# Performance work log

Measured on AMD Instinct MI355X. Metric: run time of the kernel, lower is better.

The kernel has to match this reference:

```python
import jax, jax.numpy as jnp
import numpy as np

E = 2048
H = 16
D = E // H  # head_dim = 128
S_SLOTS = 8
EPS = 1e-5


def _linear_params(key, fan_in, fan_out):
    kw, kb = jax.random.split(key)
    lim = 1.0 / np.sqrt(fan_in)
    W = jax.random.uniform(kw, (fan_out, fan_in), jnp.float32, -lim, lim)
    b = jax.random.uniform(kb, (fan_out,), jnp.float32, -lim, lim)
    return W, b


def setup_inputs() -> dict:
    key = jax.random.key(0)
    ks = jax.random.split(key, 10)
    x = jax.random.normal(ks[0], (2, 2048, E), jnp.float32)
    thought_slots = jax.random.normal(ks[1], (S_SLOTS, E), jnp.float32)
    Wq, bq = _linear_params(ks[2], E, E)
    Wk, bk = _linear_params(ks[3], E, E)
    Wv, bv = _linear_params(ks[4], E, E)
    Wtq, btq = _linear_params(ks[5], E, E)
    Wtk, btk = _linear_params(ks[6], E, E)
    Wtv, btv = _linear_params(ks[7], E, E)
    Wo, bo = _linear_params(ks[8], E, E)
    gamma = jnp.ones((E,), jnp.float32)
    beta = jnp.zeros((E,), jnp.float32)
    return dict(x=x, thought_slots=thought_slots, Wq=Wq, bq=bq, Wk=Wk, bk=bk,
                Wv=Wv, bv=bv, Wtq=Wtq, btq=btq, Wtk=Wtk, btk=btk,
                Wtv=Wtv, btv=btv, Wo=Wo, bo=bo, gamma=gamma, beta=beta)


def _heads(t, B):
    # [B, S, E] -> [B, H, S, D]
    return t.reshape(B, -1, H, D).transpose(0, 2, 1, 3)


def reference(x, thought_slots, Wq, bq, Wk, bk, Wv, bv,
              Wtq, btq, Wtk, btk, Wtv, btv, Wo, bo, gamma, beta):
    B, S, _ = x.shape
    scale = 1.0 / np.sqrt(D)

    # regular self-attention stream
    q = _heads(x @ Wq.T + bq, B)
    k = _heads(x @ Wk.T + bk, B)
    v = _heads(x @ Wv.T + bv, B)
    attn = jax.nn.softmax(jnp.einsum('bhqd,bhkd->bhqk', q, k) * scale, axis=-1)
    regular_out = jnp.einsum('bhqk,bhkd->bhqd', attn, v)

    # thought cross-attention stream (keys/values from learned slots)
    slots = jnp.broadcast_to(thought_slots, (B, S_SLOTS, thought_slots.shape[-1]))
    t_q = _heads(x @ Wtq.T + btq, B)
    t_k = _heads(slots @ Wtk.T + btk, B)
    t_v = _heads(slots @ Wtv.T + btv, B)
    t_attn = jax.nn.softmax(jnp.einsum('bhqd,bhkd->bhqk', t_q, t_k) * scale, axis=-1)
    thought_out = jnp.einsum('bhqk,bhkd->bhqd', t_attn, t_v)

    # merge heads, combine, layernorm, output projection
    combined = (regular_out + thought_out).transpose(0, 2, 1, 3).reshape(B, S, E)
    mu = jnp.mean(combined, axis=-1, keepdims=True)
    var = jnp.var(combined, axis=-1, keepdims=True)
    normed = (combined - mu) * jax.lax.rsqrt(var + EPS) * gamma + beta
    return normed @ Wo.T + bo
```

## Files before the change

### kernel.cpp

```cpp
#include <hip/hip_runtime.h>
#include <hip/hip_bf16.h>
#include <stdint.h>

typedef __bf16 bf16;
typedef __bf16 bf16x8 __attribute__((ext_vector_type(8)));
typedef __bf16 bf16x4 __attribute__((ext_vector_type(4)));
typedef float f32x4 __attribute__((ext_vector_type(4)));
typedef float f32x16 __attribute__((ext_vector_type(16)));
typedef uint32_t u32x2 __attribute__((ext_vector_type(2)));
typedef uint32_t u32x4 __attribute__((ext_vector_type(4)));

#define E_DIM 2048
#define HEADS 16
#define HD 128
#define SEQ 2048
#define BATCH 2
#define NTOK 4096
#define NSLOT 8

#define QSCALE (0.08838834764831845f * 1.4426950408889634f)

#define WAITV(N) asm volatile("s_waitcnt vmcnt(" #N ")" ::: "memory")

__device__ __forceinline__ void gload_lds16(const void* g, void* lds) {
  __builtin_amdgcn_global_load_lds(
      (const __attribute__((address_space(1))) uint32_t*)g,
      (__attribute__((address_space(3))) uint32_t*)lds, 16, 0, 0);
}

__global__ __launch_bounds__(256) void cvt_f32_bf16_kernel(
    const float* __restrict__ src, bf16* __restrict__ dst, int n8)
{
  for (int i = blockIdx.x * 256 + threadIdx.x; i < n8; i += gridDim.x * 256) {
    const f32x4 a = *(const f32x4*)(src + i * 8);
    const f32x4 b = *(const f32x4*)(src + i * 8 + 4);
    bf16x8 o;
#pragma unroll
    for (int j = 0; j < 4; j++) { o[j] = (bf16)a[j]; o[4 + j] = (bf16)b[j]; }
    *(bf16x8*)(dst + i * 8) = o;
  }
}

struct CvtArgs { const float* src[5]; bf16* dst[5]; };

__global__ __launch_bounds__(256) void cvt5_kernel(CvtArgs a, int n8)
{
  const float* __restrict__ src = a.src[blockIdx.y];
  bf16* __restrict__ dst = a.dst[blockIdx.y];
  for (int i = blockIdx.x * 256 + threadIdx.x; i < n8; i += gridDim.x * 256) {
    const f32x4 x = *(const f32x4*)(src + i * 8);
    const f32x4 y = *(const f32x4*)(src + i * 8 + 4);
    bf16x8 o;
#pragma unroll
    for (int j = 0; j < 4; j++) { o[j] = (bf16)x[j]; o[4 + j] = (bf16)y[j]; }
    *(bf16x8*)(dst + i * 8) = o;
  }
}

struct ProjArgs {
  const bf16* W[4];
  const float* bias[4];
  void* out[4];
  int mode[4];
  float scale[4];
};

__global__ __launch_bounds__(512, 2) void gemm256_kernel(
    const bf16* __restrict__ A, ProjArgs pa, int nbm, int nbn)
{
  __shared__ char As_[2 * 32768];
  __shared__ char Bs_[2 * 32768];

  const int nwg = gridDim.x;
  const int qch = nwg >> 3;
  const int wg = (blockIdx.x & 7) * qch + (blockIdx.x >> 3);
  const int bm = wg % nbm;
  const int rest = wg / nbm;
  const int bn = rest % nbn;
  const int z = rest / nbn;

  const bf16* __restrict__ W = pa.W[z];
  const float* __restrict__ bias = pa.bias[z];
  void* __restrict__ out = pa.out[z];
  const int mode = pa.mode[z];
  const float scale = pa.scale[z];

  const int tid = threadIdx.x;
  const int lane = tid & 63;
  const int w = tid >> 6;
  const int wr = w >> 2;
  const int wc = w & 3;
  const int g = lane >> 4, c = lane & 15;

  const int srow = tid >> 3;
  const int sslot = tid & 7;
  const int scol = (sslot ^ (srow & 7)) * 8;
  const bf16* Abase = A + (size_t)(bm * 256) * 2048;
  const bf16* Bbase = W + (size_t)(bn * 256) * 2048;

  auto stageU = [&](const bf16* gbase, char* lds, int T, int u) {
    char* dst = lds + (T & 1) * 32768 + u * 16384;
    const int k0 = T * 64;
#pragma unroll
    for (int j = 0; j < 2; j++) {
      const int r = u * 128 + srow + j * 64;
      gload_lds16(gbase + (size_t)r * 2048 + k0 + scol,
                  dst + (size_t)(srow + j * 64) * 128 + sslot * 16);
    }
  };

  f32x4 acc[8][4] = {};
  bf16x8 bfr[4][2];

  stageU(Bbase, Bs_, 0, 0); stageU(Bbase, Bs_, 0, 1);
  stageU(Abase, As_, 0, 0); stageU(Abase, As_, 0, 1);
  stageU(Bbase, Bs_, 1, 0); stageU(Bbase, Bs_, 1, 1);
  stageU(Abase, As_, 1, 0);
  WAITV(6);
  __builtin_amdgcn_s_barrier();

  const int NT = 2048 / 64;
  for (int t = 0; t < NT; t++) {
    const int d = t & 1;
    const char* Aq = As_ + d * 32768;
    const char* Bq = Bs_ + d * 32768;
#pragma unroll
    for (int q = 0; q < 4; q++) {
      bf16x8 af[2][2];
      if (q == 0) {
#pragma unroll
        for (int n = 0; n < 4; n++)
#pragma unroll
          for (int kk = 0; kk < 2; kk++) {
            const int row = wc * 64 + n * 16 + c;
            bfr[n][kk] = *(const bf16x8*)(Bq + (size_t)row * 128 +
                                          (((kk * 4 + g) ^ (c & 7)) * 16));
          }
      }
#pragma unroll
      for (int mi2 = 0; mi2 < 2; mi2++)
#pragma unroll
        for (int kk = 0; kk < 2; kk++) {
          const int row = wr * 128 + (q * 2 + mi2) * 16 + c;
          af[mi2][kk] = *(const bf16x8*)(Aq + (size_t)row * 128 +
                                         (((kk * 4 + g) ^ (c & 7)) * 16));
        }

      if (q == 0)      { if (t + 1 < NT) stageU(Abase, As_, t + 1, 1); }
      else if (q == 1) { if (t + 2 < NT) stageU(Bbase, Bs_, t + 2, 0); }
      else if (q == 2) { if (t + 2 < NT) stageU(Bbase, Bs_, t + 2, 1); }
      else {
        __builtin_amdgcn_s_barrier();
        if (t + 2 < NT) stageU(Abase, As_, t + 2, 0);
      }

      __builtin_amdgcn_s_setprio(1);
#pragma unroll
      for (int mi2 = 0; mi2 < 2; mi2++)
#pragma unroll
        for (int n = 0; n < 4; n++)
#pragma unroll
          for (int kk = 0; kk < 2; kk++)
            acc[q * 2 + mi2][n] = __builtin_amdgcn_mfma_f32_16x16x32_bf16(
                af[mi2][kk], bfr[n][kk], acc[q * 2 + mi2][n], 0, 0, 0);
      __builtin_amdgcn_s_setprio(0);

      if (q == 0) {
        __builtin_amdgcn_s_barrier();
      } else if (q == 3) {
        if (t < NT - 2)       { WAITV(6); }
        else if (t == NT - 2) { WAITV(0); }
        __builtin_amdgcn_s_barrier();
      }
    }
  }

#pragma unroll
  for (int mi = 0; mi < 8; mi++) {
#pragma unroll
    for (int n = 0; n < 4; n++) {
      const int col = bn * 256 + wc * 64 + n * 16 + c;
      const float bv = bias[col];
#pragma unroll
      for (int j = 0; j < 4; j++) {
        const int row = bm * 256 + wr * 128 + mi * 16 + g * 4 + j;
        const float v = (acc[mi][n][j] + bv) * scale;
        if (mode == 0) {
          ((float*)out)[(size_t)row * E_DIM + col] = v;
        } else {
          const int b = row >> 11, s = row & 2047;
          const int h = col >> 7, d2 = col & 127;
          size_t idx;
          if (mode == 1) idx = (((size_t)(b * HEADS + h)) * SEQ + s) * HD + d2;
          else           idx = (((size_t)(b * HEADS + h)) * HD + d2) * SEQ + s;
          ((bf16*)out)[idx] = (bf16)v;
        }
      }
    }
  }
}

__global__ __launch_bounds__(256) void gemm_nt_kernel(
    const bf16* __restrict__ A, ProjArgs pa, int M, int N, int K)
{
  __shared__ bf16 As[2][128 * 32];
  __shared__ bf16 Bs[2][128 * 32];

  const int z = blockIdx.z;
  const bf16* __restrict__ W = pa.W[z];
  const float* __restrict__ bias = pa.bias[z];
  void* __restrict__ out = pa.out[z];
  const int mode = pa.mode[z];
  const float scale = pa.scale[z];

  const int tid = threadIdx.x;
  const int lane = tid & 63;
  const int w = tid >> 6;
  const int wr = w >> 1, wc = w & 1;
  const int g = lane >> 4, c = lane & 15;
  const int bm = blockIdx.x, bn = blockIdx.y;

  f32x4 acc[4][4] = {};

  const int srow = lane >> 2;
  const int scol = (lane & 3) * 8;
  const bf16* Ab = A + (size_t)(bm * 128 + srow) * K + scol;
  const bf16* Wb = W + (size_t)(bn * 128 + srow) * K + scol;

  auto stage = [&](int k0, int buf) {
#pragma unroll
    for (int i = 0; i < 2; ++i) {
      const int chunk = w * 2 + i;
      gload_lds16(Ab + (size_t)(chunk * 16) * K + k0, (char*)(&As[buf][0]) + chunk * 1024);
      gload_lds16(Wb + (size_t)(chunk * 16) * K + k0, (char*)(&Bs[buf][0]) + chunk * 1024);
    }
  };

  stage(0, 0);
  __syncthreads();
  int cur = 0;

  for (int k0 = 0; k0 < K; k0 += 32) {
    if (k0 + 32 < K) stage(k0 + 32, cur ^ 1);
    bf16x8 af[4], bfr[4];
#pragma unroll
    for (int m = 0; m < 4; m++)
      af[m] = *(const bf16x8*)(&As[cur][0] + (wr * 64 + m * 16 + c) * 32 + g * 8);
#pragma unroll
    for (int n = 0; n < 4; n++)
      bfr[n] = *(const bf16x8*)(&Bs[cur][0] + (wc * 64 + n * 16 + c) * 32 + g * 8);
#pragma unroll
    for (int m = 0; m < 4; m++)
#pragma unroll
      for (int n = 0; n < 4; n++)
        acc[m][n] = __builtin_amdgcn_mfma_f32_16x16x32_bf16(af[m], bfr[n], acc[m][n], 0, 0, 0);
    __syncthreads();
    cur ^= 1;
  }

#pragma unroll
  for (int m = 0; m < 4; m++) {
#pragma unroll
    for (int n = 0; n < 4; n++) {
      const int col = bn * 128 + wc * 64 + n * 16 + c;
      const float bv = bias[col];
#pragma unroll
      for (int j = 0; j < 4; j++) {
        const int row = bm * 128 + wr * 64 + m * 16 + g * 4 + j;
        const float v = (acc[m][n][j] + bv) * scale;
        if (mode == 0) {
          ((float*)out)[(size_t)row * N + col] = v;
        } else {
          const int b = row >> 11, s = row & 2047;
          const int h = col >> 7, d = col & 127;
          size_t idx;
          if (mode == 1) idx = (((size_t)(b * HEADS + h)) * SEQ + s) * HD + d;
          else           idx = (((size_t)(b * HEADS + h)) * HD + d) * SEQ + s;
          ((bf16*)out)[idx] = (bf16)v;
        }
      }
    }
  }
}

__global__ __launch_bounds__(256) void slots_proj_kernel(
    const float* __restrict__ slots,
    const float* __restrict__ Wk, const float* __restrict__ bk,
    const float* __restrict__ Wv, const float* __restrict__ bv,
    float* __restrict__ tk, float* __restrict__ tv)
{
  const int col = blockIdx.x * 256 + threadIdx.x;
  const int slot = blockIdx.y;
  const int mat = blockIdx.z;
  const float* W = mat ? Wv : Wk;
  const float* bias = mat ? bv : bk;
  float* out = mat ? tv : tk;
  const float* xr = slots + (size_t)slot * E_DIM;
  const float* wr = W + (size_t)col * E_DIM;
  float acc = 0.f;
  for (int k = 0; k < E_DIM; k += 4) {
    const f32x4 a = *(const f32x4*)(xr + k);
    const f32x4 b4 = *(const f32x4*)(wr + k);
#pragma unroll
    for (int i = 0; i < 4; i++) acc += a[i] * b4[i];
  }
  out[(size_t)slot * E_DIM + col] = acc + bias[col];
}

__global__ __launch_bounds__(512) void flash_attn_kernel(
    const bf16* __restrict__ Qg, const bf16* __restrict__ Kg,
    const bf16* __restrict__ Vtg, bf16* __restrict__ Og)
{
  __shared__ char Ks[3][64 * 256];
  __shared__ char Vs[3][128 * 128];

  const int orig = blockIdx.x;
  const int logical = (orig & 7) * 32 + (orig >> 3);
  const int qt = logical & 7;
  const int bh = logical >> 3;

  const int tid = threadIdx.x;
  const int lane = tid & 63;
  const int w = tid >> 6;
  const int q = lane & 31;
  const int hi = lane >> 5;
  const int b = bh >> 4, h = bh & 15;
  const int q0 = qt * 256 + w * 32;

  const bf16* Qb = Qg + ((size_t)bh * SEQ + q0) * HD;
  const bf16* Kb = Kg + (size_t)bh * SEQ * HD;
  const bf16* Vb = Vtg + (size_t)bh * HD * SEQ;

  auto stage = [&](int kv0, int buf) {
#pragma unroll
    for (int i = 0; i < 2; i++) {
      const int p = (tid + i * 512) * 16;
      { const int r = p >> 8; const int s16 = (p >> 4) & 15;
        gload_lds16(Kb + (size_t)(kv0 + r) * HD + (s16 ^ (r & 15)) * 8, &Ks[0][0] + buf * 16384 + p); }
      { const int r = p >> 7; const int s8 = (p >> 4) & 7;
        gload_lds16(Vb + (size_t)r * SEQ + kv0 + (s8 ^ (r & 7)) * 8, &Vs[0][0] + buf * 16384 + p); }
    }
  };

  bf16x8 qf[8];
#pragma unroll
  for (int kc = 0; kc < 8; kc++)
    qf[kc] = *(const bf16x8*)(Qb + (size_t)q * HD + kc * 16 + hi * 8);

  f32x16 o[4] = {};
  float mrun = -1e30f, lsum = 0.f;
  bf16x8 pbo[2][2];

  stage(0, 0);
  __syncthreads();

  int prv = 2, cur = 0, nxt = 1;
  const int NT = SEQ / 64;

  for (int t = 0; t < NT; t++) {
    if (t + 1 < NT) stage((t + 1) * 64, nxt);

    f32x16 st[2] = {};
    const char* Kc = &Ks[0][0] + cur * 16384;
    __builtin_amdgcn_s_setprio(1);
#pragma unroll
    for (int kc = 0; kc < 8; kc++) {
#pragma unroll
      for (int blk = 0; blk < 2; blk++) {
        const int rt = blk * 32 + q;
        const int sl = (2 * kc + hi) ^ (rt & 15);
        const bf16x8 kf = *(const bf16x8*)(Kc + rt * 256 + sl * 16);
        st[blk] = __builtin_amdgcn_mfma_f32_32x32x16_bf16(kf, qf[kc], st[blk], 0, 0, 0);
      }
    }
    __builtin_amdgcn_s_setprio(0);

    float tm[16];
#pragma unroll
    for (int i = 0; i < 16; i++) tm[i] = fmaxf(st[0][i], st[1][i]);
#pragma unroll
    for (int s2 = 8; s2 > 0; s2 >>= 1)
#pragma unroll
      for (int i = 0; i < 8; i++) if (i < s2) tm[i] = fmaxf(tm[i], tm[i + s2]);
    float lm = tm[0];
    lm = fmaxf(lm, __shfl_xor(lm, 32));
    float fsc = 1.0f;
    const bool resc = __any(lm > mrun + 8.0f);
    if (resc) {
      const float mn = fmaxf(mrun, lm);
      fsc = exp2f(mrun - mn);
      mrun = mn;
    }

    float ps0 = 0.f, ps1 = 0.f, ps2 = 0.f, ps3 = 0.f;
#pragma unroll
    for (int blk = 0; blk < 2; blk++)
#pragma unroll
      for (int i = 0; i < 16; i += 4) {
        const float p0 = exp2f(st[blk][i]     - mrun);
        const float p1 = exp2f(st[blk][i + 1] - mrun);
        const float p2 = exp2f(st[blk][i + 2] - mrun);
        const float p3 = exp2f(st[blk][i + 3] - mrun);
        st[blk][i] = p0; st[blk][i + 1] = p1; st[blk][i + 2] = p2; st[blk][i + 3] = p3;
        ps0 += p0; ps1 += p1; ps2 += p2; ps3 += p3;
      }
    lsum = lsum * fsc + ((ps0 + ps1) + (ps2 + ps3));

    bf16x8 pbn[2][2];
#pragma unroll
    for (int blk = 0; blk < 2; blk++)
#pragma unroll
      for (int c2 = 0; c2 < 2; c2++) {
        bf16x4 Lv, Hv;
#pragma unroll
        for (int i = 0; i < 4; i++) {
          Lv[i] = (bf16)st[blk][8 * c2 + i];
          Hv[i] = (bf16)st[blk][8 * c2 + 4 + i];
        }
        const u32x2 Lu = __builtin_bit_cast(u32x2, Lv);
        const u32x2 Hu = __builtin_bit_cast(u32x2, Hv);
        const uint32_t s0 = hi ? Lu.x : Hu.x;
        const uint32_t s1 = hi ? Lu.y : Hu.y;
        const uint32_t x0 = (uint32_t)__shfl_xor((int)s0, 32);
        const uint32_t x1 = (uint32_t)__shfl_xor((int)s1, 32);
        u32x4 bv;
        bv.x = hi ? x0 : Lu.x;
        bv.y = hi ? x1 : Lu.y;
        bv.z = hi ? Hu.x : x0;
        bv.w = hi ? Hu.y : x1;
        pbn[blk][c2] = __builtin_bit_cast(bf16x8, bv);
      }

    if (t > 0) {
      const char* Vc = &Vs[0][0] + prv * 16384;
#pragma unroll
      for (int db = 0; db < 4; db++) {
        const int rt = db * 32 + q;
#pragma unroll
        for (int blk = 0; blk < 2; blk++)
#pragma unroll
          for (int c2 = 0; c2 < 2; c2++) {
            const int sl = (blk * 4 + c2 * 2 + hi) ^ (rt & 7);
            const bf16x8 vf = *(const bf16x8*)(Vc + rt * 128 + sl * 16);
            o[db] = __builtin_amdgcn_mfma_f32_32x32x16_bf16(vf, pbo[blk][c2], o[db], 0, 0, 0);
          }
      }
    }

    if (resc) {
#pragma unroll
      for (int db = 0; db < 4; db++)
#pragma unroll
        for (int i = 0; i < 16; i++) o[db][i] *= fsc;
    }

#pragma unroll
    for (int blk = 0; blk < 2; blk++)
#pragma unroll
      for (int c2 = 0; c2 < 2; c2++) pbo[blk][c2] = pbn[blk][c2];

    __syncthreads();
    const int tmp = prv; prv = cur; cur = nxt; nxt = tmp;
  }

  {
    const char* Vc = &Vs[0][0] + prv * 16384;
#pragma unroll
    for (int db = 0; db < 4; db++) {
      const int rt = db * 32 + q;
#pragma unroll
      for (int blk = 0; blk < 2; blk++)
#pragma unroll
        for (int c2 = 0; c2 < 2; c2++) {
          const int sl = (blk * 4 + c2 * 2 + hi) ^ (rt & 7);
          const bf16x8 vf = *(const bf16x8*)(Vc + rt * 128 + sl * 16);
          o[db] = __builtin_amdgcn_mfma_f32_32x32x16_bf16(vf, pbo[blk][c2], o[db], 0, 0, 0);
        }
    }
  }

  const float lt = lsum + __shfl_xor(lsum, 32);
  const float linv = 1.0f / lt;
  bf16* Orow = Og + ((size_t)b * SEQ + q0 + q) * E_DIM + h * HD;
#pragma unroll
  for (int db = 0; db < 4; db++)
#pragma unroll
    for (int g4 = 0; g4 < 4; g4++) {
      bf16x4 ov;
#pragma unroll
      for (int i = 0; i < 4; i++) ov[i] = (bf16)(o[db][g4 * 4 + i] * linv);
      *(bf16x4*)(Orow + db * 32 + g4 * 8 + hi * 4) = ov;
    }
}

__global__ __launch_bounds__(256) void thought_ln_kernel(
    const bf16* __restrict__ TQ, const float* __restrict__ TK,
    const float* __restrict__ TV, const bf16* __restrict__ ATT,
    const float* __restrict__ gamma, const float* __restrict__ beta,
    bf16* __restrict__ Y)
{
  __shared__ float wsum[4], wsq[4];
  const int tid = threadIdx.x;
  const int lane = tid & 63;
  const int w = tid >> 6;
  const int tok = blockIdx.x;
  const int b = tok >> 11, s = tok & 2047;
  const int e0 = tid * 8;
  const int h = e0 >> 7;
  const int d0 = e0 & 127;

  const bf16x8 av = *(const bf16x8*)(ATT + (size_t)tok * E_DIM + e0);
  float v[8];
#pragma unroll
  for (int i = 0; i < 8; i++) v[i] = (float)av[i];

  const bf16x8 qv8 = *(const bf16x8*)(TQ + (((size_t)(b * HEADS + h)) * SEQ + s) * HD + d0);
  float qv[8];
#pragma unroll
  for (int i = 0; i < 8; i++) qv[i] = (float)qv8[i];

  float dts[NSLOT];
#pragma unroll
  for (int sl = 0; sl < NSLOT; sl++) {
    const float* tkr = TK + (size_t)sl * E_DIM + e0;
    const f32x4 k0 = *(const f32x4*)(tkr);
    const f32x4 k1 = *(const f32x4*)(tkr + 4);
    float dp = 0.f;
#pragma unroll
    for (int i = 0; i < 4; i++) dp += qv[i] * k0[i] + qv[4 + i] * k1[i];
    dp += __shfl_xor(dp, 1);
    dp += __shfl_xor(dp, 2);
    dp += __shfl_xor(dp, 4);
    dp += __shfl_xor(dp, 8);
    dts[sl] = dp;
  }
  float mx = dts[0];
#pragma unroll
  for (int sl = 1; sl < NSLOT; sl++) mx = fmaxf(mx, dts[sl]);
  float p[NSLOT], den = 0.f;
#pragma unroll
  for (int sl = 0; sl < NSLOT; sl++) { p[sl] = exp2f(dts[sl] - mx); den += p[sl]; }
  const float dinv = 1.0f / den;
#pragma unroll
  for (int sl = 0; sl < NSLOT; sl++) {
    const float pn = p[sl] * dinv;
    const float* tvr = TV + (size_t)sl * E_DIM + e0;
    const f32x4 v0 = *(const f32x4*)(tvr);
    const f32x4 v1 = *(const f32x4*)(tvr + 4);
#pragma unroll
    for (int i = 0; i < 4; i++) { v[i] += pn * v0[i]; v[4 + i] += pn * v1[i]; }
  }

  float sm = 0.f, sq = 0.f;
#pragma unroll
  for (int i = 0; i < 8; i++) { sm += v[i]; sq += v[i] * v[i]; }
#pragma unroll
  for (int d = 1; d < 64; d <<= 1) { sm += __shfl_xor(sm, d); sq += __shfl_xor(sq, d); }
  if (lane == 0) { wsum[w] = sm; wsq[w] = sq; }
  __syncthreads();
  const float ts = wsum[0] + wsum[1] + wsum[2] + wsum[3];
  const float tq2 = wsq[0] + wsq[1] + wsq[2] + wsq[3];
  const float mean = ts * (1.f / E_DIM);
  const float var = tq2 * (1.f / E_DIM) - mean * mean;
  const float rstd = rsqrtf(var + 1e-5f);
  const f32x4 g0 = *(const f32x4*)(gamma + e0);
  const f32x4 g1 = *(const f32x4*)(gamma + e0 + 4);
  const f32x4 b0 = *(const f32x4*)(beta + e0);
  const f32x4 b1 = *(const f32x4*)(beta + e0 + 4);
  bf16x8 outv;
#pragma unroll
  for (int i = 0; i < 4; i++) {
    outv[i]     = (bf16)((v[i]     - mean) * rstd * g0[i] + b0[i]);
    outv[4 + i] = (bf16)((v[4 + i] - mean) * rstd * g1[i] + b1[i]);
  }
  *(bf16x8*)(Y + (size_t)tok * E_DIM + e0) = outv;
}

extern "C" void kernel_launch(void* const* d_in, const int* in_sizes, int n_in,
                              void* d_out, int out_size, void* d_ws, size_t ws_size,
                              hipStream_t stream) {
  (void)in_sizes; (void)n_in; (void)out_size; (void)ws_size;
  const float* x     = (const float*)d_in[0];
  const float* slots = (const float*)d_in[1];
  const float* Wq  = (const float*)d_in[2];   const float* bq  = (const float*)d_in[3];
  const float* Wk  = (const float*)d_in[4];   const float* bk  = (const float*)d_in[5];
  const float* Wv  = (const float*)d_in[6];   const float* bv  = (const float*)d_in[7];
  const float* Wtq = (const float*)d_in[8];   const float* btq = (const float*)d_in[9];
  const float* Wtk = (const float*)d_in[10];  const float* btk = (const float*)d_in[11];
  const float* Wtv = (const float*)d_in[12];  const float* btv = (const float*)d_in[13];
  const float* Wo  = (const float*)d_in[14];  const float* bo  = (const float*)d_in[15];
  const float* gamma = (const float*)d_in[16];
  const float* beta  = (const float*)d_in[17];

  uint8_t* ws = (uint8_t*)d_ws;
  const size_t BUF  = (size_t)NTOK * E_DIM * sizeof(bf16);
  const size_t WBUF = (size_t)E_DIM * E_DIM * sizeof(bf16);
  bf16* xb   = (bf16*)(ws + 0 * BUF);
  bf16* qb   = (bf16*)(ws + 1 * BUF);
  bf16* kb   = (bf16*)(ws + 2 * BUF);
  bf16* vtb  = (bf16*)(ws + 3 * BUF);
  bf16* tqb  = (bf16*)(ws + 4 * BUF);
  bf16* attb = (bf16*)(ws + 5 * BUF);
  bf16* nrmb = qb;
  uint8_t* wp = ws + 6 * BUF;
  bf16* Wqb  = (bf16*)(wp + 0 * WBUF);
  bf16* Wkb  = (bf16*)(wp + 1 * WBUF);
  bf16* Wvb  = (bf16*)(wp + 2 * WBUF);
  bf16* Wtqb = (bf16*)(wp + 3 * WBUF);
  bf16* Wob  = (bf16*)(wp + 4 * WBUF);
  float* tkb = (float*)(wp + 5 * WBUF);
  float* tvb = (float*)(wp + 5 * WBUF + 128 * 1024);

  const int WN8 = E_DIM * E_DIM / 8;
  const int XN8 = NTOK * E_DIM / 8;
  cvt_f32_bf16_kernel<<<dim3(2048), 256, 0, stream>>>(x, xb, XN8);
  CvtArgs ca;
  ca.src[0] = Wq;  ca.dst[0] = Wqb;
  ca.src[1] = Wk;  ca.dst[1] = Wkb;
  ca.src[2] = Wv;  ca.dst[2] = Wvb;
  ca.src[3] = Wtq; ca.dst[3] = Wtqb;
  ca.src[4] = Wo;  ca.dst[4] = Wob;
  cvt5_kernel<<<dim3(1024, 5), 256, 0, stream>>>(ca, WN8);

  ProjArgs pa;
  pa.W[0] = Wqb;  pa.bias[0] = bq;  pa.out[0] = qb;  pa.mode[0] = 1; pa.scale[0] = QSCALE;
  pa.W[1] = Wkb;  pa.bias[1] = bk;  pa.out[1] = kb;  pa.mode[1] = 1; pa.scale[1] = 1.0f;
  pa.W[2] = Wvb;  pa.bias[2] = bv;  pa.out[2] = vtb; pa.mode[2] = 2; pa.scale[2] = 1.0f;
  pa.W[3] = Wtqb; pa.bias[3] = btq; pa.out[3] = tqb; pa.mode[3] = 1; pa.scale[3] = QSCALE;
  gemm256_kernel<<<dim3(16 * 8 * 4), 512, 0, stream>>>(xb, pa, 16, 8);

  slots_proj_kernel<<<dim3(E_DIM / 256, NSLOT, 2), 256, 0, stream>>>(
      slots, Wtk, btk, Wtv, btv, tkb, tvb);

  flash_attn_kernel<<<dim3((SEQ / 256) * BATCH * HEADS), 512, 0, stream>>>(
      qb, kb, vtb, attb);
  thought_ln_kernel<<<dim3(NTOK), 256, 0, stream>>>(
      tqb, tkb, tvb, attb, gamma, beta, nrmb);

  ProjArgs po;
  po.W[0] = Wob; po.bias[0] = bo; po.out[0] = d_out; po.mode[0] = 0; po.scale[0] = 1.0f;
  po.W[1] = po.W[2] = po.W[3] = Wob;
  po.bias[1] = po.bias[2] = po.bias[3] = bo;
  po.out[1] = po.out[2] = po.out[3] = d_out;
  po.mode[1] = po.mode[2] = po.mode[3] = 0;
  po.scale[1] = po.scale[2] = po.scale[3] = 1.0f;
  gemm_nt_kernel<<<dim3(NTOK / 128, E_DIM / 128, 1), 256, 0, stream>>>(
      nrmb, po, NTOK, E_DIM, E_DIM);
}
```

Baseline: 432.0 us.

## Replace output projection with split-K 256-tile GEMM and bias reduction

The output projection no longer uses the small 128x128-tile GEMM. It now runs a 256x256-tile kernel with split-K of 2 over 256 workgroups, remapped across XCDs. Each half writes bf16 partials into reused workspace buffers, and a separate kernel sums them, adds the bias and writes the fp32 output. The A-tile staging order and LDS layout are also changed, and the barrier placement is adjusted in the main QKV GEMM loop. The aim is better MFMA utilisation and more occupancy for the last GEMM, at the cost of an extra partial round-trip through memory and bf16 rounding of the partials.

```diff
diff --git a/kernel.cpp b/kernel.cpp
--- a/kernel.cpp
+++ b/kernel.cpp
@@ -98,13 +98,23 @@
   const bf16* Abase = A + (size_t)(bm * 256) * 2048;
   const bf16* Bbase = W + (size_t)(bn * 256) * 2048;
 
-  auto stageU = [&](const bf16* gbase, char* lds, int T, int u) {
-    char* dst = lds + (T & 1) * 32768 + u * 16384;
+  auto stageB = [&](int T, int u) {
+    char* dst = Bs_ + (T & 1) * 32768 + u * 16384;
     const int k0 = T * 64;
 #pragma unroll
     for (int j = 0; j < 2; j++) {
       const int r = u * 128 + srow + j * 64;
-      gload_lds16(gbase + (size_t)r * 2048 + k0 + scol,
+      gload_lds16(Bbase + (size_t)r * 2048 + k0 + scol,
+                  dst + (size_t)(srow + j * 64) * 128 + sslot * 16);
+    }
+  };
+  auto stageA = [&](int T, int u) {
+    char* dst = As_ + (T & 1) * 32768 + u * 16384;
+    const int k0 = T * 64;
+#pragma unroll
+    for (int j = 0; j < 2; j++) {
+      const int r = j * 128 + u * 64 + srow;
+      gload_lds16(Abase + (size_t)r * 2048 + k0 + scol,
                   dst + (size_t)(srow + j * 64) * 128 + sslot * 16);
     }
   };
@@ -112,10 +122,8 @@
   f32x4 acc[8][4] = {};
   bf16x8 bfr[4][2];
 
-  stageU(Bbase, Bs_, 0, 0); stageU(Bbase, Bs_, 0, 1);
-  stageU(Abase, As_, 0, 0); stageU(Abase, As_, 0, 1);
-  stageU(Bbase, Bs_, 1, 0); stageU(Bbase, Bs_, 1, 1);
-  stageU(Abase, As_, 1, 0);
+  stageB(0, 0); stageB(0, 1); stageA(0, 0); stageA(0, 1);
+  stageB(1, 0); stageB(1, 1); stageA(1, 0);
   WAITV(6);
   __builtin_amdgcn_s_barrier();
 
@@ -142,17 +150,15 @@
 #pragma unroll
         for (int kk = 0; kk < 2; kk++) {
           const int row = wr * 128 + (q * 2 + mi2) * 16 + c;
-          af[mi2][kk] = *(const bf16x8*)(Aq + (size_t)row * 128 +
+          const int slab = (row >> 6) & 1;
+          const int aoff = (row & 63) + ((row >> 7) << 6);
+          af[mi2][kk] = *(const bf16x8*)(Aq + slab * 16384 + (size_t)aoff * 128 +
                                          (((kk * 4 + g) ^ (c & 7)) * 16));
         }
 
-      if (q == 0)      { if (t + 1 < NT) stageU(Abase, As_, t + 1, 1); }
-      else if (q == 1) { if (t + 2 < NT) stageU(Bbase, Bs_, t + 2, 0); }
-      else if (q == 2) { if (t + 2 < NT) stageU(Bbase, Bs_, t + 2, 1); }
-      else {
-        __builtin_amdgcn_s_barrier();
-        if (t + 2 < NT) stageU(Abase, As_, t + 2, 0);
-      }
+      if (q == 0)      { if (t + 1 < NT) stageA(t + 1, 1); }
+      else if (q == 2) { if (t + 2 < NT) stageB(t + 2, 0); }
+      else if (q == 3) { if (t + 2 < NT) { stageB(t + 2, 1); stageA(t + 2, 0); } }
 
       __builtin_amdgcn_s_setprio(1);
 #pragma unroll
@@ -165,7 +171,7 @@
                 af[mi2][kk], bfr[n][kk], acc[q * 2 + mi2][n], 0, 0, 0);
       __builtin_amdgcn_s_setprio(0);
 
-      if (q == 0) {
+      if (q == 1) {
         __builtin_amdgcn_s_barrier();
       } else if (q == 3) {
         if (t < NT - 2)       { WAITV(6); }
@@ -185,101 +191,162 @@
       for (int j = 0; j < 4; j++) {
         const int row = bm * 256 + wr * 128 + mi * 16 + g * 4 + j;
         const float v = (acc[mi][n][j] + bv) * scale;
-        if (mode == 0) {
-          ((float*)out)[(size_t)row * E_DIM + col] = v;
-        } else {
-          const int b = row >> 11, s = row & 2047;
-          const int h = col >> 7, d2 = col & 127;
-          size_t idx;
-          if (mode == 1) idx = (((size_t)(b * HEADS + h)) * SEQ + s) * HD + d2;
-          else           idx = (((size_t)(b * HEADS + h)) * HD + d2) * SEQ + s;
-          ((bf16*)out)[idx] = (bf16)v;
-        }
-      }
-    }
-  }
-}
-
-__global__ __launch_bounds__(256) void gemm_nt_kernel(
-    const bf16* __restrict__ A, ProjArgs pa, int M, int N, int K)
+        const int b = row >> 11, s = row & 2047;
+        const int h = col >> 7, d2 = col & 127;
+        size_t idx;
+        if (mode == 1) idx = (((size_t)(b * HEADS + h)) * SEQ + s) * HD + d2;
+        else           idx = (((size_t)(b * HEADS + h)) * HD + d2) * SEQ + s;
+        ((bf16*)out)[idx] = (bf16)v;
+      }
+    }
+  }
+}
+
+__global__ __launch_bounds__(512, 2) void gemm256k_kernel(
+    const bf16* __restrict__ A, const bf16* __restrict__ W,
+    bf16* __restrict__ P0, bf16* __restrict__ P1)
 {
-  __shared__ bf16 As[2][128 * 32];
-  __shared__ bf16 Bs[2][128 * 32];
-
-  const int z = blockIdx.z;
-  const bf16* __restrict__ W = pa.W[z];
-  const float* __restrict__ bias = pa.bias[z];
-  void* __restrict__ out = pa.out[z];
-  const int mode = pa.mode[z];
-  const float scale = pa.scale[z];
+  __shared__ char As_[2 * 32768];
+  __shared__ char Bs_[2 * 32768];
+
+  const int nwg = gridDim.x;
+  const int qch = nwg >> 3;
+  const int wg = (blockIdx.x & 7) * qch + (blockIdx.x >> 3);
+  const int bm = wg % 16;
+  const int rest = wg / 16;
+  const int bn = rest & 7;
+  const int ks = rest >> 3;
+  bf16* __restrict__ out = ks ? P1 : P0;
+  const int kbase = ks * 1024;
 
   const int tid = threadIdx.x;
   const int lane = tid & 63;
   const int w = tid >> 6;
-  const int wr = w >> 1, wc = w & 1;
+  const int wr = w >> 2;
+  const int wc = w & 3;
   const int g = lane >> 4, c = lane & 15;
-  const int bm = blockIdx.x, bn = blockIdx.y;
-
-  f32x4 acc[4][4] = {};
-
-  const int srow = lane >> 2;
-  const int scol = (lane & 3) * 8;
-  const bf16* Ab = A + (size_t)(bm * 128 + srow) * K + scol;
-  const bf16* Wb = W + (size_t)(bn * 128 + srow) * K + scol;
-
-  auto stage = [&](int k0, int buf) {
-#pragma unroll
-    for (int i = 0; i < 2; ++i) {
-      const int chunk = w * 2 + i;
-      gload_lds16(Ab + (size_t)(chunk * 16) * K + k0, (char*)(&As[buf][0]) + chunk * 1024);
-      gload_lds16(Wb + (size_t)(chunk * 16) * K + k0, (char*)(&Bs[buf][0]) + chunk * 1024);
+
+  const int srow = tid >> 3;
+  const int sslot = tid & 7;
+  const int scol = (sslot ^ (srow & 7)) * 8;
+  const bf16* Abase = A + (size_t)(bm * 256) * 2048;
+  const bf16* Bbase = W + (size_t)(bn * 256) * 2048;
+
+  auto stageB = [&](int T, int u) {
+    char* dst = Bs_ + (T & 1) * 32768 + u * 16384;
+    const int k0 = kbase + T * 64;
+#pragma unroll
+    for (int j = 0; j < 2; j++) {
+      const int r = u * 128 + srow + j * 64;
+      gload_lds16(Bbase + (size_t)r * 2048 + k0 + scol,
+                  dst + (size_t)(srow + j * 64) * 128 + sslot * 16);
     }
   };
-
-  stage(0, 0);
-  __syncthreads();
-  int cur = 0;
-
-  for (int k0 = 0; k0 < K; k0 += 32) {
-    if (k0 + 32 < K) stage(k0 + 32, cur ^ 1);
-    bf16x8 af[4], bfr[4];
-#pragma unroll
-    for (int m = 0; m < 4; m++)
-      af[m] = *(const bf16x8*)(&As[cur][0] + (wr * 64 + m * 16 + c) * 32 + g * 8);
-#pragma unroll
-    for (int n = 0; n < 4; n++)
-      bfr[n] = *(const bf16x8*)(&Bs[cur][0] + (wc * 64 + n * 16 + c) * 32 + g * 8);
-#pragma unroll
-    for (int m = 0; m < 4; m++)
-#pragma unroll
-      for (int n = 0; n < 4; n++)
-        acc[m][n] = __builtin_amdgcn_mfma_f32_16x16x32_bf16(af[m], bfr[n], acc[m][n], 0, 0, 0);
-    __syncthreads();
-    cur ^= 1;
-  }
-
-#pragma unroll
-  for (int m = 0; m < 4; m++) {
+  auto stageA = [&](int T, int u) {
+    char* dst = As_ + (T & 1) * 32768 + u * 16384;
+    const int k0 = kbase + T * 64;
+#pragma unroll
+    for (int j = 0; j < 2; j++) {
+      const int r = j * 128 + u * 64 + srow;
+      gload_lds16(Abase + (size_t)r * 2048 + k0 + scol,
+                  dst + (size_t)(srow + j * 64) * 128 + sslot * 16);
+    }
+  };
+
+  f32x4 acc[8][4] = {};
+  bf16x8 bfr[4][2];
+
+  stageB(0, 0); stageB(0, 1); stageA(0, 0); stageA(0, 1);
+  stageB(1, 0); stageB(1, 1); stageA(1, 0);
+  WAITV(6);
+  __builtin_amdgcn_s_barrier();
+
+  const int NT = 16;
+  for (int t = 0; t < NT; t++) {
+    const int d = t & 1;
+    const char* Aq = As_ + d * 32768;
+    const char* Bq = Bs_ + d * 32768;
+#pragma unroll
+    for (int q = 0; q < 4; q++) {
+      bf16x8 af[2][2];
+      if (q == 0) {
+#pragma unroll
+        for (int n = 0; n < 4; n++)
+#pragma unroll
+          for (int kk = 0; kk < 2; kk++) {
+            const int row = wc * 64 + n * 16 + c;
+            bfr[n][kk] = *(const bf16x8*)(Bq + (size_t)row * 128 +
+                                          (((kk * 4 + g) ^ (c & 7)) * 16));
+          }
+      }
+#pragma unroll
+      for (int mi2 = 0; mi2 < 2; mi2++)
+#pragma unroll
+        for (int kk = 0; kk < 2; kk++) {
+          const int row = wr * 128 + (q * 2 + mi2) * 16 + c;
+          const int slab = (row >> 6) & 1;
+          const int aoff = (row & 63) + ((row >> 7) << 6);
+          af[mi2][kk] = *(const bf16x8*)(Aq + slab * 16384 + (size_t)aoff * 128 +
+                                         (((kk * 4 + g) ^ (c & 7)) * 16));
+        }
+
+      if (q == 0)      { if (t + 1 < NT) stageA(t + 1, 1); }
+      else if (q == 2) { if (t + 2 < NT) stageB(t + 2, 0); }
+      else if (q == 3) { if (t + 2 < NT) { stageB(t + 2, 1); stageA(t + 2, 0); } }
+
+      __builtin_amdgcn_s_setprio(1);
+#pragma unroll
+      for (int mi2 = 0; mi2 < 2; mi2++)
+#pragma unroll
+        for (int n = 0; n < 4; n++)
+#pragma unroll
+          for (int kk = 0; kk < 2; kk++)
+            acc[q * 2 + mi2][n] = __builtin_amdgcn_mfma_f32_16x16x32_bf16(
+                af[mi2][kk], bfr[n][kk], acc[q * 2 + mi2][n], 0, 0, 0);
+      __builtin_amdgcn_s_setprio(0);
+
+      if (q == 1) {
+        __builtin_amdgcn_s_barrier();
+      } else if (q == 3) {
+        if (t < NT - 2)       { WAITV(6); }
+        else if (t == NT - 2) { WAITV(0); }
+        __builtin_amdgcn_s_barrier();
+      }
+    }
+  }
+
+#pragma unroll
+  for (int mi = 0; mi < 8; mi++) {
 #pragma unroll
     for (int n = 0; n < 4; n++) {
-      const int col = bn * 128 + wc * 64 + n * 16 + c;
-      const float bv = bias[col];
+      const int col = bn * 256 + wc * 64 + n * 16 + c;
 #pragma unroll
       for (int j = 0; j < 4; j++) {
-        const int row = bm * 128 + wr * 64 + m * 16 + g * 4 + j;
-        const float v = (acc[m][n][j] + bv) * scale;
-        if (mode == 0) {
-          ((float*)out)[(size_t)row * N + col] = v;
-        } else {
-          const int b = row >> 11, s = row & 2047;
-          const int h = col >> 7, d = col & 127;
-          size_t idx;
-          if (mode == 1) idx = (((size_t)(b * HEADS + h)) * SEQ + s) * HD + d;
-          else           idx = (((size_t)(b * HEADS + h)) * HD + d) * SEQ + s;
-          ((bf16*)out)[idx] = (bf16)v;
-        }
-      }
-    }
+        const int row = bm * 256 + wr * 128 + mi * 16 + g * 4 + j;
+        out[(size_t)row * E_DIM + col] = (bf16)acc[mi][n][j];
+      }
+    }
+  }
+}
+
+__global__ __launch_bounds__(256) void reduce_bias_kernel(
+    const bf16* __restrict__ P0, const bf16* __restrict__ P1,
+    const float* __restrict__ bias, float* __restrict__ out, int n8)
+{
+  for (int i = blockIdx.x * 256 + threadIdx.x; i < n8; i += gridDim.x * 256) {
+    const bf16x8 a = *(const bf16x8*)(P0 + (size_t)i * 8);
+    const bf16x8 b = *(const bf16x8*)(P1 + (size_t)i * 8);
+    const int col = (i * 8) & 2047;
+    const f32x4 b0 = *(const f32x4*)(bias + col);
+    const f32x4 b1 = *(const f32x4*)(bias + col + 4);
+    f32x4 o0, o1;
+#pragma unroll
+    for (int j = 0; j < 4; j++) {
+      o0[j] = (float)a[j] + (float)b[j] + b0[j];
+      o1[j] = (float)a[4 + j] + (float)b[4 + j] + b1[j];
+    }
+    *(f32x4*)(out + (size_t)i * 8) = o0;
+    *(f32x4*)(out + (size_t)i * 8 + 4) = o1;
   }
 }
 
@@ -602,6 +669,8 @@
   bf16* tqb  = (bf16*)(ws + 4 * BUF);
   bf16* attb = (bf16*)(ws + 5 * BUF);
   bf16* nrmb = qb;
+  bf16* P0   = kb;
+  bf16* P1   = vtb;
   uint8_t* wp = ws + 6 * BUF;
   bf16* Wqb  = (bf16*)(wp + 0 * WBUF);
   bf16* Wkb  = (bf16*)(wp + 1 * WBUF);
@@ -637,13 +706,7 @@
   thought_ln_kernel<<<dim3(NTOK), 256, 0, stream>>>(
       tqb, tkb, tvb, attb, gamma, beta, nrmb);
 
-  ProjArgs po;
-  po.W[0] = Wob; po.bias[0] = bo; po.out[0] = d_out; po.mode[0] = 0; po.scale[0] = 1.0f;
-  po.W[1] = po.W[2] = po.W[3] = Wob;
-  po.bias[1] = po.bias[2] = po.bias[3] = bo;
-  po.out[1] = po.out[2] = po.out[3] = d_out;
-  po.mode[1] = po.mode[2] = po.mode[3] = 0;
-  po.scale[1] = po.scale[2] = po.scale[3] = 1.0f;
-  gemm_nt_kernel<<<dim3(NTOK / 128, E_DIM / 128, 1), 256, 0, stream>>>(
-      nrmb, po, NTOK, E_DIM, E_DIM);
-}
+  gemm256k_kernel<<<dim3(256), 512, 0, stream>>>(nrmb, Wob, P0, P1);
+  reduce_bias_kernel<<<dim3(2048), 256, 0, stream>>>(
+      P0, P1, bo, (float*)d_out, NTOK * E_DIM / 8);
+}
```

New measurement: 427.2 us, median of 2. No clear change (-1.1%).
